# Performance work log

Measured on AMD Instinct MI355X. Metric: run time of the kernel, lower is better.

## Reference

```python
import jax, jax.numpy as jnp
import numpy as np

PROCESSING_SPEED = 8.0  # init kwarg: softmax temperature
EPS = 1e-8              # torch F.cosine_similarity eps
BATCH, SIZE, DIM = 1024, 65536, 512


def setup_inputs() -> dict:
    key = jax.random.key(0)
    k1, k2 = jax.random.split(key)
    x = jax.random.normal(k1, (BATCH, DIM), dtype=jnp.float32)
    memory_bank = jax.random.normal(k2, (SIZE, DIM), dtype=jnp.float32)
    return {"x": x, "memory_bank": memory_bank}


def reference(x, memory_bank):
    # Cosine similarity between every query and every memory row, computed as
    # normalized dot products (math-equivalent to F.cosine_similarity with
    # denominator clamp max(||a||*||b||, eps), avoiding the (B,S,D) broadcast).
    x_norm = jnp.linalg.norm(x, axis=1, keepdims=True)            # (B, 1)
    m_norm = jnp.linalg.norm(memory_bank, axis=1, keepdims=True)  # (S, 1)
    dots = jnp.einsum('bd,sd->bs', x, memory_bank)                # (B, S)
    sims = dots / jnp.maximum(x_norm * m_norm.T, EPS)             # (B, S)
    attention = jax.nn.softmax(sims * PROCESSING_SPEED, axis=1)   # (B, S)
    return attention @ memory_bank                                # (B, D)
```

## Files before the change

kernel.cpp:

```cpp
#include <hip/hip_runtime.h>
#include <hip/hip_bf16.h>
#include <stdint.h>

#define B_N 1024
#define S_N 65536
#define D_N 512
#define NS 32
#define SC (S_N / NS)
#define SB 128
#define NSUB (SC / SB)

typedef __attribute__((ext_vector_type(8))) short bf16x8;
typedef __attribute__((ext_vector_type(4))) float f32x4;

#define OFF_MBF   ((size_t)0)
#define OFF_MT    (OFF_MBF + (size_t)S_N * D_N * 2)
#define OFF_XBF   (OFF_MT  + (size_t)D_N * S_N * 2)
#define OFF_RX    (OFF_XBF + (size_t)B_N * D_N * 2)
#define OFF_RM    (OFF_RX  + (size_t)B_N * 4)
#define OFF_LSUM  (OFF_RM  + (size_t)S_N * 4)
#define OFF_OPART (OFF_LSUM + (size_t)B_N * 4)

__device__ __forceinline__ unsigned short f2bf(float f) {
  unsigned u = __builtin_bit_cast(unsigned, f);
  u += 0x7fffu + ((u >> 16) & 1u);
  return (unsigned short)(u >> 16);
}

__device__ __forceinline__ void stage16(const unsigned short* g, unsigned short* l) {
  __builtin_amdgcn_global_load_lds(
      (const __attribute__((address_space(1))) void*)g,
      (__attribute__((address_space(3))) void*)l, 16, 0, 0);
}

__global__ void k_prep_x(const float* __restrict__ X, unsigned short* __restrict__ Xbf,
                         float* __restrict__ rx) {
  const int row = blockIdx.x;
  const int t = threadIdx.x;
  float4 v = ((const float4*)(X + (size_t)row * D_N))[t];
  float ss = v.x*v.x + v.y*v.y + v.z*v.z + v.w*v.w;
  ushort4 o; o.x = f2bf(v.x); o.y = f2bf(v.y); o.z = f2bf(v.z); o.w = f2bf(v.w);
  ((ushort4*)(Xbf + (size_t)row * D_N))[t] = o;
  #pragma unroll
  for (int m = 1; m < 64; m <<= 1) ss += __shfl_xor(ss, m);
  __shared__ float partial[2];
  if ((t & 63) == 0) partial[t >> 6] = ss;
  __syncthreads();
  if (t == 0) rx[row] = 11.541560327111707f * rsqrtf(fmaxf(partial[0] + partial[1], 1e-24f));
}

__global__ void k_prep_m(const float* __restrict__ M, unsigned short* __restrict__ Mbf,
                         unsigned short* __restrict__ Mt, float* __restrict__ rm) {
  __shared__ float ts[64 * 65];
  const int t = threadIdx.x;
  const int s0 = blockIdx.x * 64;
  const int r = t >> 2, cq = t & 3;
  const int c = t >> 2, sq = t & 3;
  float ss = 0.f;
  for (int ct = 0; ct < 8; ++ct) {
    float f[16];
    const float4* src = (const float4*)(M + (size_t)(s0 + r) * D_N + ct * 64 + cq * 16);
    #pragma unroll
    for (int k = 0; k < 4; ++k) {
      float4 v = src[k];
      f[4*k+0] = v.x; f[4*k+1] = v.y; f[4*k+2] = v.z; f[4*k+3] = v.w;
    }
    union { unsigned short u[16]; uint4 v4[2]; } pk;
    #pragma unroll
    for (int j = 0; j < 16; ++j) {
      ss += f[j] * f[j];
      pk.u[j] = f2bf(f[j]);
      ts[r * 65 + cq * 16 + j] = f[j];
    }
    uint4* dst = (uint4*)(Mbf + (size_t)(s0 + r) * D_N + ct * 64 + cq * 16);
    dst[0] = pk.v4[0]; dst[1] = pk.v4[1];
    __syncthreads();
    union { unsigned short u[16]; uint4 v4[2]; } pt;
    #pragma unroll
    for (int j = 0; j < 16; ++j) pt.u[j] = f2bf(ts[(sq * 16 + j) * 65 + c]);
    uint4* dt = (uint4*)(Mt + (size_t)(ct * 64 + c) * S_N + s0 + sq * 16);
    dt[0] = pt.v4[0]; dt[1] = pt.v4[1];
    __syncthreads();
  }
  ss += __shfl_xor(ss, 1);
  ss += __shfl_xor(ss, 2);
  if (cq == 0) rm[s0 + r] = rsqrtf(fmaxf(ss, 1e-24f));
}

__global__ __launch_bounds__(512, 2) void k_fused(
    const unsigned short* __restrict__ Xbf, const unsigned short* __restrict__ Mbf,
    const unsigned short* __restrict__ Mt, const float* __restrict__ rx,
    const float* __restrict__ rminv, float* __restrict__ lsum,
    float* __restrict__ Opart) {
  __shared__ unsigned short sbuf[2][16384];
  __shared__ unsigned short Ps[16384];

  const int t = threadIdx.x;
  const int w = t >> 6, lane = t & 63, quad = lane >> 4, l15 = lane & 15;
  const int qr = w >> 1, qc = w & 1;
  const int x7 = l15 & 7;

  const int bid = blockIdx.x;
  const int xcd = bid & 7, slot = bid >> 3;
  const int bblk = slot & 7;
  const int chunk = xcd * 4 + (slot >> 3);
  const int b0 = bblk * 128;
  const int s0 = chunk * SC;

  f32x4 accO[4][2][4];
  #pragma unroll
  for (int dc = 0; dc < 4; ++dc)
    #pragma unroll
    for (int i = 0; i < 2; ++i)
      #pragma unroll
      for (int j = 0; j < 4; ++j) accO[dc][i][j] = (f32x4){0.f, 0.f, 0.f, 0.f};

  float ls[4] = {0.f, 0.f, 0.f, 0.f};
  float rxj[4];
  #pragma unroll
  for (int j = 0; j < 4; ++j) rxj[j] = rx[b0 + qc * 64 + j * 16 + l15];

  const int srow8 = t >> 3;
  const int sch8  = ((t & 7) ^ (srow8 & 7)) * 8;
  const unsigned short* gX0 = Xbf + (size_t)(b0 + srow8) * D_N + sch8;
  const unsigned short* gM0 = Mbf + (size_t)srow8 * D_N + sch8;
  const int mrow = t >> 4;
  const int mch  = ((t & 15) ^ (mrow & 7)) * 8;
  const unsigned short* gT0 = Mt + (size_t)mrow * S_N + mch;

  #define ISSUE_QK(sS_, k0_, bi_) do {                                       \
    unsigned short* bA_ = &sbuf[(bi_)][0];                                   \
    unsigned short* bB_ = &sbuf[(bi_)][8192];                                \
    const unsigned short* gM_ = gM0 + (size_t)(sS_) * D_N + (k0_);           \
    stage16(gM_,                   bA_ + w * 512);                           \
    stage16(gM_ + (size_t)64*D_N,  bA_ + 4096 + w * 512);                    \
    const unsigned short* gX_ = gX0 + (k0_);                                 \
    stage16(gX_,                   bB_ + w * 512);                           \
    stage16(gX_ + (size_t)64*D_N,  bB_ + 4096 + w * 512);                    \
  } while (0)

  #define ISSUE_PV(sS_, dc_, bi_) do {                                       \
    unsigned short* bT_ = &sbuf[(bi_)][0];                                   \
    const unsigned short* gT_ = gT0 + (size_t)((dc_) * 128) * S_N + (sS_);   \
    stage16(gT_,                   bT_ + w * 512);                           \
    stage16(gT_ + (size_t)32*S_N,  bT_ + 4096 + w * 512);                    \
    stage16(gT_ + (size_t)64*S_N,  bT_ + 8192 + w * 512);                    \
    stage16(gT_ + (size_t)96*S_N,  bT_ + 12288 + w * 512);                   \
  } while (0)

  ISSUE_QK(s0, 0, 0);

  for (int sub = 0; sub < NSUB; ++sub) {
    const int sS = s0 + sub * SB;

    f32x4 accP[2][4];
    #pragma unroll
    for (int i = 0; i < 2; ++i)
      #pragma unroll
      for (int j = 0; j < 4; ++j) accP[i][j] = (f32x4){0.f, 0.f, 0.f, 0.f};

    #pragma unroll
    for (int st = 0; st < 8; ++st) {
      const int bi = st & 1;
      if (st < 7) { ISSUE_QK(sS, (st + 1) * 64, bi ^ 1); }
      else        { ISSUE_PV(sS, 0, bi ^ 1); }
      asm volatile("s_waitcnt vmcnt(4)" ::: "memory");
      __builtin_amdgcn_s_barrier();
      const unsigned short* As = &sbuf[bi][0];
      const unsigned short* Bs = &sbuf[bi][8192];
      __builtin_amdgcn_s_setprio(1);
      #pragma unroll
      for (int kk = 0; kk < 64; kk += 32) {
        const int cq = (kk >> 3) + quad;
        bf16x8 a[2], b[4];
        #pragma unroll
        for (int i = 0; i < 2; ++i)
          a[i] = *(const bf16x8*)&As[(qr * 32 + i * 16 + l15) * 64 + ((cq ^ x7) << 3)];
        #pragma unroll
        for (int j = 0; j < 4; ++j)
          b[j] = *(const bf16x8*)&Bs[(qc * 64 + j * 16 + l15) * 64 + ((cq ^ x7) << 3)];
        #pragma unroll
        for (int i = 0; i < 2; ++i)
          #pragma unroll
          for (int j = 0; j < 4; ++j)
            accP[i][j] = __builtin_amdgcn_mfma_f32_16x16x32_bf16(a[i], b[j], accP[i][j], 0, 0, 0);
      }
      __builtin_amdgcn_s_setprio(0);
      __builtin_amdgcn_s_barrier();
    }

    {
      const float4 rm0 = *(const float4*)&rminv[sS + qr * 32 + quad * 4];
      const float4 rm1 = *(const float4*)&rminv[sS + qr * 32 + 16 + quad * 4];
      #pragma unroll
      for (int i = 0; i < 2; ++i) {
        const float4 rm = i ? rm1 : rm0;
        const int sl  = qr * 32 + i * 16 + quad * 4;
        const int c16 = sl >> 3;
        const int o8  = (sl >> 2) & 1;
        #pragma unroll
        for (int j = 0; j < 4; ++j) {
          const float p0 = exp2f(accP[i][j][0] * rxj[j] * rm.x);
          const float p1 = exp2f(accP[i][j][1] * rxj[j] * rm.y);
          const float p2 = exp2f(accP[i][j][2] * rxj[j] * rm.z);
          const float p3 = exp2f(accP[i][j][3] * rxj[j] * rm.w);
          ls[j] += (p0 + p1) + (p2 + p3);
          const int brow = qc * 64 + j * 16 + l15;
          uint2 pk;
          pk.x = (unsigned)f2bf(p0) | ((unsigned)f2bf(p1) << 16);
          pk.y = (unsigned)f2bf(p2) | ((unsigned)f2bf(p3) << 16);
          *(uint2*)&Ps[brow * 128 + (((c16 ^ (brow & 7)) << 3) | (o8 << 2))] = pk;
        }
      }
      asm volatile("s_waitcnt lgkmcnt(0)" ::: "memory");
    }

    #pragma unroll
    for (int dc = 0; dc < 4; ++dc) {
      const int bi = dc & 1;
      if (dc < 3)                  { ISSUE_PV(sS, dc + 1, bi ^ 1); }
      else if (sub < NSUB - 1)     { ISSUE_QK(sS + SB, 0, bi ^ 1); }
      if (dc == 3 && sub == NSUB - 1) asm volatile("s_waitcnt vmcnt(0)" ::: "memory");
      else                            asm volatile("s_waitcnt vmcnt(4)" ::: "memory");
      __builtin_amdgcn_s_barrier();
      const unsigned short* Tsb = &sbuf[bi][0];
      __builtin_amdgcn_s_setprio(1);
      #pragma unroll
      for (int kk = 0; kk < 128; kk += 32) {
        const int cq = (kk >> 3) + quad;
        bf16x8 pa[2], mb[4];
        #pragma unroll
        for (int i = 0; i < 2; ++i)
          pa[i] = *(const bf16x8*)&Ps[(qr * 32 + i * 16 + l15) * 128 + ((cq ^ x7) << 3)];
        #pragma unroll
        for (int j = 0; j < 4; ++j)
          mb[j] = *(const bf16x8*)&Tsb[(qc * 64 + j * 16 + l15) * 128 + ((cq ^ x7) << 3)];
        #pragma unroll
        for (int i = 0; i < 2; ++i)
          #pragma unroll
          for (int j = 0; j < 4; ++j)
            accO[dc][i][j] = __builtin_amdgcn_mfma_f32_16x16x32_bf16(pa[i], mb[j], accO[dc][i][j], 0, 0, 0);
      }
      __builtin_amdgcn_s_setprio(0);
      __builtin_amdgcn_s_barrier();
    }
  }

  float* Od = Opart + (size_t)chunk * ((size_t)B_N * D_N);
  #pragma unroll
  for (int dc = 0; dc < 4; ++dc)
    #pragma unroll
    for (int i = 0; i < 2; ++i)
      #pragma unroll
      for (int r = 0; r < 4; ++r) {
        const int bb = b0 + qr * 32 + i * 16 + quad * 4 + r;
        #pragma unroll
        for (int j = 0; j < 4; ++j) {
          const int d = dc * 128 + qc * 64 + j * 16 + l15;
          Od[(size_t)bb * D_N + d] = accO[dc][i][j][r];
        }
      }

  __syncthreads();
  float* red = (float*)&sbuf[0][0];
  #pragma unroll
  for (int j = 0; j < 4; ++j) {
    float v = ls[j];
    v += __shfl_xor(v, 16);
    v += __shfl_xor(v, 32);
    if (lane < 16) red[w * 64 + j * 16 + lane] = v;
  }
  __syncthreads();
  if (t < 128) {
    const int qc2 = t >> 6, idx = t & 63;
    float s = red[(0 + qc2) * 64 + idx] + red[(2 + qc2) * 64 + idx] +
              red[(4 + qc2) * 64 + idx] + red[(6 + qc2) * 64 + idx];
    unsafeAtomicAdd(&lsum[b0 + t], s);
  }
  #undef ISSUE_QK
  #undef ISSUE_PV
}

__global__ void k_combine(const float* __restrict__ Opart, const float* __restrict__ lsum,
                          float* __restrict__ out) {
  const int idx = blockIdx.x * 256 + threadIdx.x;
  const int b = idx >> 7;
  float4 s = {0.f, 0.f, 0.f, 0.f};
  #pragma unroll
  for (int ks = 0; ks < NS; ++ks) {
    float4 v = ((const float4*)Opart)[(size_t)ks * (B_N * D_N / 4) + idx];
    s.x += v.x; s.y += v.y; s.z += v.z; s.w += v.w;
  }
  const float inv = 1.0f / lsum[b];
  s.x *= inv; s.y *= inv; s.z *= inv; s.w *= inv;
  ((float4*)out)[idx] = s;
}

extern "C" void kernel_launch(void* const* d_in, const int* in_sizes, int n_in,
                              void* d_out, int out_size, void* d_ws, size_t ws_size,
                              hipStream_t stream) {
  const float* X = (const float*)d_in[0];
  const float* M = (const float*)d_in[1];
  char* ws = (char*)d_ws;
  unsigned short* Mbf = (unsigned short*)(ws + OFF_MBF);
  unsigned short* Mt  = (unsigned short*)(ws + OFF_MT);
  unsigned short* Xbf = (unsigned short*)(ws + OFF_XBF);
  float* rxv  = (float*)(ws + OFF_RX);
  float* rmv  = (float*)(ws + OFF_RM);
  float* lsum = (float*)(ws + OFF_LSUM);
  float* Opart = (float*)(ws + OFF_OPART);

  hipMemsetAsync(lsum, 0, B_N * sizeof(float), stream);
  k_prep_x<<<dim3(B_N), 128, 0, stream>>>(X, Xbf, rxv);
  k_prep_m<<<dim3(S_N / 64), 256, 0, stream>>>(M, Mbf, Mt, rmv);
  k_fused<<<dim3(8 * NS), 512, 0, stream>>>(Xbf, Mbf, Mt, rxv, rmv, lsum, Opart);
  k_combine<<<dim3(B_N * D_N / 4 / 256), 256, 0, stream>>>(Opart, lsum, (float*)d_out);
}
```

Before: 429.6 us.

## Triple-buffer staging with prefetch distance two and pad P tile stride

Expands the LDS staging ring from two to three slots. Global loads are now issued two stages ahead, after the barrier, which removes the trailing barrier from every QK and PV stage. The P tile in shared memory switches from an XOR-swizzled 128-element row to a padded 136-element stride, which simplifies its address math. In exchange the kernel uses more LDS, which limits occupancy, and the bank-conflict behaviour of the P writes and reads changes.

```diff
diff --git a/kernel.cpp b/kernel.cpp
--- a/kernel.cpp
+++ b/kernel.cpp
@@ -9,6 +9,7 @@
 #define SC (S_N / NS)
 #define SB 128
 #define NSUB (SC / SB)
+#define PSTRIDE 136
 
 typedef __attribute__((ext_vector_type(8))) short bf16x8;
 typedef __attribute__((ext_vector_type(4))) float f32x4;
@@ -92,8 +93,8 @@
     const unsigned short* __restrict__ Mt, const float* __restrict__ rx,
     const float* __restrict__ rminv, float* __restrict__ lsum,
     float* __restrict__ Opart) {
-  __shared__ unsigned short sbuf[2][16384];
-  __shared__ unsigned short Ps[16384];
+  __shared__ unsigned short sbuf[3][16384];
+  __shared__ unsigned short Ps[128 * PSTRIDE];
 
   const int t = threadIdx.x;
   const int w = t >> 6, lane = t & 63, quad = lane >> 4, l15 = lane & 15;
@@ -128,9 +129,9 @@
   const int mch  = ((t & 15) ^ (mrow & 7)) * 8;
   const unsigned short* gT0 = Mt + (size_t)mrow * S_N + mch;
 
-  #define ISSUE_QK(sS_, k0_, bi_) do {                                       \
-    unsigned short* bA_ = &sbuf[(bi_)][0];                                   \
-    unsigned short* bB_ = &sbuf[(bi_)][8192];                                \
+  #define ISSUE_QK(sS_, k0_, sl_) do {                                       \
+    unsigned short* bA_ = &sbuf[(sl_)][0];                                   \
+    unsigned short* bB_ = &sbuf[(sl_)][8192];                                \
     const unsigned short* gM_ = gM0 + (size_t)(sS_) * D_N + (k0_);           \
     stage16(gM_,                   bA_ + w * 512);                           \
     stage16(gM_ + (size_t)64*D_N,  bA_ + 4096 + w * 512);                    \
@@ -139,8 +140,8 @@
     stage16(gX_ + (size_t)64*D_N,  bB_ + 4096 + w * 512);                    \
   } while (0)
 
-  #define ISSUE_PV(sS_, dc_, bi_) do {                                       \
-    unsigned short* bT_ = &sbuf[(bi_)][0];                                   \
+  #define ISSUE_PV(sS_, dc_, sl_) do {                                       \
+    unsigned short* bT_ = &sbuf[(sl_)][0];                                   \
     const unsigned short* gT_ = gT0 + (size_t)((dc_) * 128) * S_N + (sS_);   \
     stage16(gT_,                   bT_ + w * 512);                           \
     stage16(gT_ + (size_t)32*S_N,  bT_ + 4096 + w * 512);                    \
@@ -149,6 +150,7 @@
   } while (0)
 
   ISSUE_QK(s0, 0, 0);
+  ISSUE_QK(s0, 64, 1);
 
   for (int sub = 0; sub < NSUB; ++sub) {
     const int sS = s0 + sub * SB;
@@ -160,14 +162,13 @@
       for (int j = 0; j < 4; ++j) accP[i][j] = (f32x4){0.f, 0.f, 0.f, 0.f};
 
     #pragma unroll
-    for (int st = 0; st < 8; ++st) {
-      const int bi = st & 1;
-      if (st < 7) { ISSUE_QK(sS, (st + 1) * 64, bi ^ 1); }
-      else        { ISSUE_PV(sS, 0, bi ^ 1); }
+    for (int ph = 0; ph < 8; ++ph) {
       asm volatile("s_waitcnt vmcnt(4)" ::: "memory");
       __builtin_amdgcn_s_barrier();
-      const unsigned short* As = &sbuf[bi][0];
-      const unsigned short* Bs = &sbuf[bi][8192];
+      if (ph < 6) { ISSUE_QK(sS, (ph + 2) * 64, (ph + 2) % 3); }
+      else        { ISSUE_PV(sS, ph - 6, (ph + 2) % 3); }
+      const unsigned short* As = &sbuf[ph % 3][0];
+      const unsigned short* Bs = &sbuf[ph % 3][8192];
       __builtin_amdgcn_s_setprio(1);
       #pragma unroll
       for (int kk = 0; kk < 64; kk += 32) {
@@ -186,7 +187,6 @@
             accP[i][j] = __builtin_amdgcn_mfma_f32_16x16x32_bf16(a[i], b[j], accP[i][j], 0, 0, 0);
       }
       __builtin_amdgcn_s_setprio(0);
-      __builtin_amdgcn_s_barrier();
     }
 
     {
@@ -195,9 +195,7 @@
       #pragma unroll
       for (int i = 0; i < 2; ++i) {
         const float4 rm = i ? rm1 : rm0;
-        const int sl  = qr * 32 + i * 16 + quad * 4;
-        const int c16 = sl >> 3;
-        const int o8  = (sl >> 2) & 1;
+        const int sl = qr * 32 + i * 16 + quad * 4;
         #pragma unroll
         for (int j = 0; j < 4; ++j) {
           const float p0 = exp2f(accP[i][j][0] * rxj[j] * rm.x);
@@ -209,7 +207,7 @@
           uint2 pk;
           pk.x = (unsigned)f2bf(p0) | ((unsigned)f2bf(p1) << 16);
           pk.y = (unsigned)f2bf(p2) | ((unsigned)f2bf(p3) << 16);
-          *(uint2*)&Ps[brow * 128 + (((c16 ^ (brow & 7)) << 3) | (o8 << 2))] = pk;
+          *(uint2*)&Ps[brow * PSTRIDE + sl] = pk;
         }
       }
       asm volatile("s_waitcnt lgkmcnt(0)" ::: "memory");
@@ -217,13 +215,12 @@
 
     #pragma unroll
     for (int dc = 0; dc < 4; ++dc) {
-      const int bi = dc & 1;
-      if (dc < 3)                  { ISSUE_PV(sS, dc + 1, bi ^ 1); }
-      else if (sub < NSUB - 1)     { ISSUE_QK(sS + SB, 0, bi ^ 1); }
       if (dc == 3 && sub == NSUB - 1) asm volatile("s_waitcnt vmcnt(0)" ::: "memory");
       else                            asm volatile("s_waitcnt vmcnt(4)" ::: "memory");
       __builtin_amdgcn_s_barrier();
-      const unsigned short* Tsb = &sbuf[bi][0];
+      if (dc < 2)                { ISSUE_PV(sS, dc + 2, (10 + dc) % 3); }
+      else if (sub < NSUB - 1)   { ISSUE_QK(sS + SB, (dc - 2) * 64, (10 + dc) % 3); }
+      const unsigned short* Tsb = &sbuf[(8 + dc) % 3][0];
       __builtin_amdgcn_s_setprio(1);
       #pragma unroll
       for (int kk = 0; kk < 128; kk += 32) {
@@ -231,7 +228,7 @@
         bf16x8 pa[2], mb[4];
         #pragma unroll
         for (int i = 0; i < 2; ++i)
-          pa[i] = *(const bf16x8*)&Ps[(qr * 32 + i * 16 + l15) * 128 + ((cq ^ x7) << 3)];
+          pa[i] = *(const bf16x8*)&Ps[(qr * 32 + i * 16 + l15) * PSTRIDE + (cq << 3)];
         #pragma unroll
         for (int j = 0; j < 4; ++j)
           mb[j] = *(const bf16x8*)&Tsb[(qc * 64 + j * 16 + l15) * 128 + ((cq ^ x7) << 3)];
@@ -242,7 +239,6 @@
             accO[dc][i][j] = __builtin_amdgcn_mfma_f32_16x16x32_bf16(pa[i], mb[j], accO[dc][i][j], 0, 0, 0);
       }
       __builtin_amdgcn_s_setprio(0);
-      __builtin_amdgcn_s_barrier();
     }
   }
 
```

Measured after the change: 433.2 us. About the same (+0.8%).
